# Kernel optimization log

Hardware: AMD Instinct MI355X
Metric: run time of the kernel (lower is better)

## Reference

```python
import jax, jax.numpy as jnp
import numpy as np

B, S, D = 8, 1024, 1024
H = 16
HD = D // H  # 64
FF = 4 * D   # 4096
EPS = 1e-5


def layer_norm(x, g, b):
    mu = jnp.mean(x, axis=-1, keepdims=True)
    var = jnp.mean(jnp.square(x - mu), axis=-1, keepdims=True)
    return (x - mu) * jax.lax.rsqrt(var + EPS) * g + b


def setup_inputs() -> dict:
    key = jax.random.key(0)
    ks = jax.random.split(key, 16)
    s_in = 1.0 / np.sqrt(D)
    s_ff = 1.0 / np.sqrt(FF)
    return {
        "x": jax.random.normal(ks[0], (B, S, D), jnp.float32),
        "ln1_g": jnp.ones((D,), jnp.float32),
        "ln1_b": jnp.zeros((D,), jnp.float32),
        "ln2_g": jnp.ones((D,), jnp.float32),
        "ln2_b": jnp.zeros((D,), jnp.float32),
        # per-head projections stacked on a leading head axis: [H, D, HD]
        "Wq": jax.random.uniform(ks[1], (H, D, HD), jnp.float32, -s_in, s_in),
        "bq": jax.random.uniform(ks[2], (H, HD), jnp.float32, -s_in, s_in),
        "Wk": jax.random.uniform(ks[3], (H, D, HD), jnp.float32, -s_in, s_in),
        "bk": jax.random.uniform(ks[4], (H, HD), jnp.float32, -s_in, s_in),
        "Wv": jax.random.uniform(ks[5], (H, D, HD), jnp.float32, -s_in, s_in),
        "bv": jax.random.uniform(ks[6], (H, HD), jnp.float32, -s_in, s_in),
        "Wo": jax.random.uniform(ks[7], (D, D), jnp.float32, -s_in, s_in),
        "bo": jax.random.uniform(ks[8], (D,), jnp.float32, -s_in, s_in),
        "W1": jax.random.uniform(ks[9], (D, FF), jnp.float32, -s_in, s_in),
        "b1": jax.random.uniform(ks[10], (FF,), jnp.float32, -s_in, s_in),
        "W2": jax.random.uniform(ks[11], (FF, D), jnp.float32, -s_ff, s_ff),
        "b2": jax.random.uniform(ks[12], (D,), jnp.float32, -s_ff, s_ff),
    }


def attention(h, Wq, bq, Wk, bk, Wv, bv, Wo, bo):
    # h: [B,S,D] -> q/k/v: [B,H,S,HD]
    q = jnp.einsum("bsd,hdk->bhsk", h, Wq) + bq[None, :, None, :]
    k = jnp.einsum("bsd,hdk->bhsk", h, Wk) + bk[None, :, None, :]
    v = jnp.einsum("bsd,hdk->bhsk", h, Wv) + bv[None, :, None, :]
    scores = jnp.einsum("bhsk,bhtk->bhst", q, k) / jnp.sqrt(jnp.float32(HD))
    w = jax.nn.softmax(scores, axis=-1)  # [B,H,S,S]
    o = jnp.einsum("bhst,bhtk->bhsk", w, v)
    # concat heads (head order matches torch.cat over per-head outputs)
    o = o.transpose(0, 2, 1, 3).reshape(h.shape[0], h.shape[1], D)
    return o @ Wo + bo


def reference(x, ln1_g, ln1_b, ln2_g, ln2_b, Wq, bq, Wk, bk, Wv, bv, Wo, bo, W1, b1, W2, b2):
    h = layer_norm(x, ln1_g, ln1_b)
    x = x + attention(h, Wq, bq, Wk, bk, Wv, bv, Wo, bo)
    h2 = layer_norm(x, ln2_g, ln2_b)
    ff = jax.nn.gelu(h2 @ W1 + b1, approximate=False) @ W2 + b2  # dropout in eval = identity
    return x + ff
```

## Files before the change

### kernel.cpp

```cpp
#include <hip/hip_runtime.h>
#include <hip/hip_bf16.h>
#include <math.h>

#define DMODEL 1024
#define NH     16
#define HD     64
#define FFDIM  4096
#define SEQ    1024
#define BATCH  8
#define ROWS   (BATCH * SEQ)

typedef __bf16 bf16x8 __attribute__((ext_vector_type(8)));
typedef __bf16 bf16x4 __attribute__((ext_vector_type(4)));
typedef float  f32x4  __attribute__((ext_vector_type(4)));
typedef short  s16x4  __attribute__((ext_vector_type(4)));
typedef unsigned int u32x2 __attribute__((ext_vector_type(2)));

__device__ __forceinline__ unsigned short f2bf(float f) {
  unsigned int u = __builtin_bit_cast(unsigned int, f);
  u += 0x7fff + ((u >> 16) & 1);
  return (unsigned short)(u >> 16);
}

__device__ __forceinline__ unsigned int cvt_pk_bf16(float lo, float hi) {
  unsigned int r;
  asm("v_cvt_pk_bf16_f32 %0, %1, %2" : "=v"(r) : "v"(lo), "v"(hi));
  return r;
}

__device__ __forceinline__ void gload_lds16(const void* g, void* l) {
  __builtin_amdgcn_global_load_lds(
      (const __attribute__((address_space(1))) unsigned int*)g,
      (__attribute__((address_space(3))) unsigned int*)l, 16, 0, 0);
}

__global__ __launch_bounds__(256) void ln_bf16_kernel(
    const float* __restrict__ x, const float* __restrict__ g,
    const float* __restrict__ bta, unsigned short* __restrict__ out) {
  int row = blockIdx.x;
  int tid = threadIdx.x;
  int wid = tid >> 6, lane = tid & 63;
  const float4 v = ((const float4*)(x + (size_t)row * DMODEL))[tid];
  float s = v.x + v.y + v.z + v.w;
#pragma unroll
  for (int off = 32; off >= 1; off >>= 1) s += __shfl_xor(s, off, 64);
  __shared__ float red[8];
  if (lane == 0) red[wid] = s;
  __syncthreads();
  float mu = (red[0] + red[1] + red[2] + red[3]) * (1.0f / DMODEL);
  float4 d;
  d.x = v.x - mu; d.y = v.y - mu; d.z = v.z - mu; d.w = v.w - mu;
  float sq = d.x * d.x + d.y * d.y + d.z * d.z + d.w * d.w;
#pragma unroll
  for (int off = 32; off >= 1; off >>= 1) sq += __shfl_xor(sq, off, 64);
  if (lane == 0) red[4 + wid] = sq;
  __syncthreads();
  float var = (red[4] + red[5] + red[6] + red[7]) * (1.0f / DMODEL);
  float rs = rsqrtf(var + 1e-5f);
  const float4 gg = ((const float4*)g)[tid];
  const float4 bb = ((const float4*)bta)[tid];
  ushort4 o;
  o.x = f2bf(d.x * rs * gg.x + bb.x);
  o.y = f2bf(d.y * rs * gg.y + bb.y);
  o.z = f2bf(d.z * rs * gg.z + bb.z);
  o.w = f2bf(d.w * rs * gg.w + bb.w);
  ((ushort4*)(out + (size_t)row * DMODEL))[tid] = o;
}

__global__ __launch_bounds__(256) void transpose_f2b_kernel(
    const float* __restrict__ in, unsigned short* __restrict__ out,
    int R, int C, long long ibs, long long obs) {
  __shared__ float tile[64][65];
  int b = blockIdx.z;
  int r0 = blockIdx.y * 64, c0 = blockIdx.x * 64;
  const float* ip = in + (size_t)b * ibs;
  unsigned short* op = out + (size_t)b * obs;
  int tid = threadIdx.x;
  int rl = tid >> 4, cl = (tid & 15) * 4;
#pragma unroll
  for (int it = 0; it < 4; ++it) {
    int r = it * 16 + rl;
    float4 v = *(const float4*)(ip + (size_t)(r0 + r) * C + c0 + cl);
    tile[r][cl] = v.x; tile[r][cl + 1] = v.y;
    tile[r][cl + 2] = v.z; tile[r][cl + 3] = v.w;
  }
  __syncthreads();
#pragma unroll
  for (int it = 0; it < 4; ++it) {
    int c = it * 16 + rl;
    ushort4 o;
    o.x = f2bf(tile[cl + 0][c]); o.y = f2bf(tile[cl + 1][c]);
    o.z = f2bf(tile[cl + 2][c]); o.w = f2bf(tile[cl + 3][c]);
    *(ushort4*)(op + (size_t)(c0 + c) * R + r0 + cl) = o;
  }
}

__global__ __launch_bounds__(256) void transpose_qkv_kernel(
    const float* __restrict__ Wq, const float* __restrict__ Wk,
    const float* __restrict__ Wv, unsigned short* __restrict__ out) {
  __shared__ float tile[64][65];
  int z = blockIdx.z;
  int wsel = z >> 4, head = z & 15;
  const float* base = (wsel == 0) ? Wq : (wsel == 1) ? Wk : Wv;
  const float* ip = base + (size_t)head * 65536;
  unsigned short* op = out + (size_t)z * 65536;
  int r0 = blockIdx.y * 64;
  int tid = threadIdx.x;
  int rl = tid >> 4, cl = (tid & 15) * 4;
#pragma unroll
  for (int it = 0; it < 4; ++it) {
    int r = it * 16 + rl;
    float4 v = *(const float4*)(ip + (size_t)(r0 + r) * 64 + cl);
    tile[r][cl] = v.x; tile[r][cl + 1] = v.y;
    tile[r][cl + 2] = v.z; tile[r][cl + 3] = v.w;
  }
  __syncthreads();
#pragma unroll
  for (int it = 0; it < 4; ++it) {
    int c = it * 16 + rl;
    ushort4 o;
    o.x = f2bf(tile[cl + 0][c]); o.y = f2bf(tile[cl + 1][c]);
    o.z = f2bf(tile[cl + 2][c]); o.w = f2bf(tile[cl + 3][c]);
    *(ushort4*)(op + (size_t)c * 1024 + r0 + cl) = o;
  }
}

__global__ __launch_bounds__(256) void transpose_v_kernel(
    const unsigned short* __restrict__ V, unsigned short* __restrict__ Vt) {
  __shared__ unsigned short tile[64][68];
  int bh = blockIdx.y;
  int b = bh >> 4, h = bh & 15;
  int t0 = blockIdx.x * 64;
  int tid = threadIdx.x;
  int rl = tid >> 4, cl = (tid & 15) * 4;
  const unsigned short* ip = V + ((size_t)(b * SEQ + t0)) * DMODEL + h * HD;
#pragma unroll
  for (int it = 0; it < 4; ++it) {
    int t = it * 16 + rl;
    ushort4 v = *(const ushort4*)(ip + (size_t)t * DMODEL + cl);
    tile[t][cl] = v.x; tile[t][cl + 1] = v.y;
    tile[t][cl + 2] = v.z; tile[t][cl + 3] = v.w;
  }
  __syncthreads();
  unsigned short* op = Vt + ((size_t)bh * HD) * SEQ + t0;
#pragma unroll
  for (int it = 0; it < 4; ++it) {
    int d = it * 16 + rl;
    ushort4 o;
    o.x = tile[cl + 0][d]; o.y = tile[cl + 1][d];
    o.z = tile[cl + 2][d]; o.w = tile[cl + 3][d];
    *(ushort4*)(op + (size_t)d * SEQ + cl) = o;
  }
}

#define QSCALE 0.18033688f

template <int EPI>
__global__ __launch_bounds__(512, 4) void gemmdb_kernel(
    const unsigned short* __restrict__ A, const unsigned short* __restrict__ Bt,
    const float* __restrict__ bias, const float* __restrict__ resid,
    unsigned short* __restrict__ outb, float* __restrict__ outf,
    int M, int N, int K, int NX) {
  __shared__ __align__(16) unsigned short As[2 * 128 * 64];
  __shared__ __align__(16) unsigned short Bs[2 * 128 * 64];

  const int tid = threadIdx.x;
  const int wid = tid >> 6, lane = tid & 63;
  const int l15 = lane & 15, l4 = lane >> 4;
  const int wm = wid >> 1, wn = wid & 1;

  const int id = (int)blockIdx.x;
  const int xcd = id & 7, j = id >> 3;
  const int w = j >> 6, l = j & 63;
  const int spx = (int)gridDim.x >> 9;
  const int nbx8 = NX >> 3;
  const int g = xcd * spx + w;
  const int by = (g / nbx8) * 8 + (l >> 3);
  const int bx = (g % nbx8) * 8 + (l & 7);

  const size_t KBY = (size_t)K * 2;

  const int rS = tid >> 3;
  const int cS = ((tid & 7) ^ (rS & 7)) << 4;
  const char* gA = (const char*)A + (size_t)(by * 128 + rS) * KBY + cS;
  const char* gB = (const char*)Bt + (size_t)(bx * 128 + rS) * KBY + cS;
  char* sA = (char*)As + tid * 16;
  char* sB = (char*)Bs + tid * 16;

  const int rsw = (l4 ^ (l15 & 7)) << 4;
  const char* aRd0 = (const char*)As + (wm * 32 + l15) * 128 + rsw;
  const char* aRd1 = (const char*)As + (wm * 32 + l15) * 128 + (rsw ^ 64);
  const char* bRd0 = (const char*)Bs + (wn * 64 + l15) * 128 + rsw;
  const char* bRd1 = (const char*)Bs + (wn * 64 + l15) * 128 + (rsw ^ 64);

  f32x4 acc[2][4];
  const f32x4 fz = {0.f, 0.f, 0.f, 0.f};
#pragma unroll
  for (int i = 0; i < 2; ++i)
#pragma unroll
    for (int j2 = 0; j2 < 4; ++j2) acc[i][j2] = fz;

  const int nt = K >> 6;

  gload_lds16(gA, sA);
  gload_lds16(gA + 64 * KBY, sA + 8192);
  gload_lds16(gB, sB);
  gload_lds16(gB + 64 * KBY, sB + 8192);
  asm volatile("s_waitcnt vmcnt(0)" ::: "memory");
  __builtin_amdgcn_sched_barrier(0);
  __builtin_amdgcn_s_barrier();
  __builtin_amdgcn_sched_barrier(0);

#pragma unroll 1
  for (int t = 0; t < nt; ++t) {
    const int cur = t & 1;
    if (t + 1 < nt) {
      const size_t ko = (size_t)(t + 1) << 7;
      const int nb = (cur ^ 1) << 14;
      gload_lds16(gA + ko, sA + nb);
      gload_lds16(gA + 64 * KBY + ko, sA + nb + 8192);
      gload_lds16(gB + ko, sB + nb);
      gload_lds16(gB + 64 * KBY + ko, sB + nb + 8192);
    }
    const int off = cur << 14;
#pragma unroll
    for (int kk = 0; kk < 2; ++kk) {
      const char* aR = (kk ? aRd1 : aRd0) + off;
      const char* bR = (kk ? bRd1 : bRd0) + off;
      bf16x8 afr[2], bfr[4];
#pragma unroll
      for (int ni = 0; ni < 4; ++ni) bfr[ni] = *(const bf16x8*)(bR + ni * 2048);
#pragma unroll
      for (int mi = 0; mi < 2; ++mi) afr[mi] = *(const bf16x8*)(aR + mi * 2048);
      __builtin_amdgcn_s_setprio(1);
#pragma unroll
      for (int mi = 0; mi < 2; ++mi)
#pragma unroll
        for (int ni = 0; ni < 4; ++ni)
          acc[mi][ni] = __builtin_amdgcn_mfma_f32_16x16x32_bf16(
              afr[mi], bfr[ni], acc[mi][ni], 0, 0, 0);
      __builtin_amdgcn_s_setprio(0);
    }
    asm volatile("s_waitcnt vmcnt(0)" ::: "memory");
    __builtin_amdgcn_sched_barrier(0);
    __builtin_amdgcn_s_barrier();
    __builtin_amdgcn_sched_barrier(0);
  }

#pragma unroll
  for (int mi = 0; mi < 2; ++mi) {
#pragma unroll
    for (int ni = 0; ni < 4; ++ni) {
      int col = bx * 128 + wn * 64 + ni * 16 + l15;
      float bn = bias[col];
#pragma unroll
      for (int jj = 0; jj < 4; ++jj) {
        int row = by * 128 + wm * 32 + mi * 16 + l4 * 4 + jj;
        float v = acc[mi][ni][jj] + bn;
        if (EPI == 1) {
          outf[(size_t)row * N + col] = v + resid[(size_t)row * N + col];
        } else {
          outb[(size_t)row * N + col] = f2bf(v);
        }
      }
    }
  }
}

template <int EPI>
__global__ __launch_bounds__(512, 2) void gemmbig_kernel(
    const unsigned short* __restrict__ A, const unsigned short* __restrict__ Bt,
    const float* __restrict__ bias, const float* __restrict__ bias2,
    const float* __restrict__ bias3,
    unsigned short* __restrict__ outb, unsigned short* __restrict__ outb2,
    unsigned short* __restrict__ outb3,
    int M, int N, int K, int YPX) {
  __shared__ __align__(16) unsigned short As[2 * 256 * 64];
  __shared__ __align__(16) unsigned short Bs[2 * 256 * 64];

  const int tid = threadIdx.x;
  const int wid = tid >> 6, lane = tid & 63;
  const int l15 = lane & 15, l4 = lane >> 4;
  const int wm = wid >> 2, wn = wid & 3;

  const int id = (int)blockIdx.x;
  const int xcd = id & 7, i0 = id >> 3;
  const int by = xcd * YPX + (i0 % YPX);
  const int bx = i0 / YPX;

  const size_t KBY = (size_t)K * 2;

  const int rS = tid >> 3;
  const int cS = ((tid & 7) ^ (rS & 7)) << 4;
  const char* gA = (const char*)A + (size_t)(by * 256 + rS) * KBY + cS;
  const char* gB = (const char*)Bt + (size_t)(bx * 256 + rS) * KBY + cS;
  char* sA = (char*)As + tid * 16;
  char* sB = (char*)Bs + tid * 16;

  const int rsw = (l4 ^ (l15 & 7)) << 4;
  const char* aRd0 = (const char*)As + (wm * 128 + l15) * 128 + rsw;
  const char* aRd1 = (const char*)As + (wm * 128 + l15) * 128 + (rsw ^ 64);
  const char* bRd0 = (const char*)Bs + (wn * 64 + l15) * 128 + rsw;
  const char* bRd1 = (const char*)Bs + (wn * 64 + l15) * 128 + (rsw ^ 64);

  f32x4 acc[8][4];
  const f32x4 fz = {0.f, 0.f, 0.f, 0.f};
#pragma unroll
  for (int i = 0; i < 8; ++i)
#pragma unroll
    for (int n = 0; n < 4; ++n) acc[i][n] = fz;

  const int nt = K >> 6;

#define STAGE8(NB, KO)                                                       \
  do {                                                                       \
    gload_lds16(gA + (KO), sA + (NB));                                       \
    gload_lds16(gA + 64 * KBY + (KO), sA + (NB) + 8192);                     \
    gload_lds16(gA + 128 * KBY + (KO), sA + (NB) + 16384);                   \
    gload_lds16(gA + 192 * KBY + (KO), sA + (NB) + 24576);                   \
    gload_lds16(gB + (KO), sB + (NB));                                       \
    gload_lds16(gB + 64 * KBY + (KO), sB + (NB) + 8192);                     \
    gload_lds16(gB + 128 * KBY + (KO), sB + (NB) + 16384);                   \
    gload_lds16(gB + 192 * KBY + (KO), sB + (NB) + 24576);                   \
  } while (0)

  STAGE8(0, 0);
  asm volatile("s_waitcnt vmcnt(0)" ::: "memory");
  __builtin_amdgcn_sched_barrier(0);
  __builtin_amdgcn_s_barrier();
  __builtin_amdgcn_sched_barrier(0);

#pragma unroll 1
  for (int t = 0; t < nt; ++t) {
    const int cur = t & 1;
    if (t + 1 < nt) STAGE8((cur ^ 1) << 15, (size_t)(t + 1) << 7);
    const int off = cur << 15;
#pragma unroll
    for (int kk = 0; kk < 2; ++kk) {
      const char* aR = (kk ? aRd1 : aRd0) + off;
      const char* bR = (kk ? bRd1 : bRd0) + off;
      bf16x8 av[8], bv[4];
#pragma unroll
      for (int ni = 0; ni < 4; ++ni) bv[ni] = *(const bf16x8*)(bR + ni * 2048);
#pragma unroll
      for (int mi = 0; mi < 8; ++mi) av[mi] = *(const bf16x8*)(aR + mi * 2048);
      __builtin_amdgcn_s_setprio(1);
#pragma unroll
      for (int mi = 0; mi < 8; ++mi)
#pragma unroll
        for (int ni = 0; ni < 4; ++ni)
          acc[mi][ni] = __builtin_amdgcn_mfma_f32_16x16x32_bf16(
              av[mi], bv[ni], acc[mi][ni], 0, 0, 0);
      __builtin_amdgcn_s_setprio(0);
    }
    asm volatile("s_waitcnt vmcnt(0)" ::: "memory");
    __builtin_amdgcn_sched_barrier(0);
    __builtin_amdgcn_s_barrier();
    __builtin_amdgcn_sched_barrier(0);
  }

  if (EPI == 5) {
    const int range = bx >> 2;
    const float* bp = (range == 0) ? bias : (range == 1) ? bias2 : bias3;
    unsigned short* op = (range == 0) ? outb : (range == 1) ? outb2 : outb3;
    const float scale = (range == 0) ? QSCALE : 1.0f;
#pragma unroll
    for (int mi = 0; mi < 8; ++mi) {
#pragma unroll
      for (int ni = 0; ni < 4; ++ni) {
        int colL = (bx & 3) * 256 + wn * 64 + ni * 16 + l15;
        float bn = bp[colL];
#pragma unroll
        for (int jj = 0; jj < 4; ++jj) {
          int row = by * 256 + wm * 128 + mi * 16 + l4 * 4 + jj;
          op[(size_t)row * 1024 + colL] = f2bf((acc[mi][ni][jj] + bn) * scale);
        }
      }
    }
  } else {
#pragma unroll
    for (int mi = 0; mi < 8; ++mi) {
#pragma unroll
      for (int ni = 0; ni < 4; ++ni) {
        int col = bx * 256 + wn * 64 + ni * 16 + l15;
        float bn = bias[col];
#pragma unroll
        for (int jj = 0; jj < 4; ++jj) {
          int row = by * 256 + wm * 128 + mi * 16 + l4 * 4 + jj;
          float v = acc[mi][ni][jj] + bn;
          float gel = 0.5f * v * (1.0f + erff(v * 0.70710678118f));
          outb[(size_t)row * N + col] = f2bf(gel);
        }
      }
    }
  }
#undef STAGE8
}

__global__ __launch_bounds__(256, 3) void attn_kernel(
    const unsigned short* __restrict__ Q, const unsigned short* __restrict__ K,
    const unsigned short* __restrict__ Vt, unsigned short* __restrict__ O) {
  __shared__ __align__(16) unsigned short Ks[128 * 64];
  __shared__ __align__(16) unsigned short Vs[64 * 128];
  int tid = threadIdx.x, wid = tid >> 6, lane = tid & 63;
  int l15 = lane & 15, l4 = lane >> 4;
  int sid = blockIdx.x;
  int aid = (sid & 7) * 256 + (sid >> 3);
  int bh = aid >> 4, qb = aid & 15;
  int b = bh >> 4, h = bh & 15;
  int q0 = qb * 64 + wid * 16;
  const f32x4 fz = {0.f, 0.f, 0.f, 0.f};

  const unsigned short* Qbase = Q + ((size_t)(b * SEQ + q0)) * DMODEL + h * HD;
  bf16x8 qf[2];
#pragma unroll
  for (int kh = 0; kh < 2; ++kh)
    qf[kh] = *(const bf16x8*)(Qbase + (size_t)l15 * DMODEL + kh * 32 + l4 * 8);

  f32x4 o[4];
#pragma unroll
  for (int i = 0; i < 4; ++i) o[i] = fz;
  float mrun = -1e30f, lrun = 0.0f;

  const unsigned short* Kb = K + (size_t)b * SEQ * DMODEL + h * HD;
  const unsigned short* Vb = Vt + (size_t)bh * HD * SEQ;
  int krow = tid >> 3, kchunk = tid & 7;
  int vrow = tid >> 4, vchunk = tid & 15;

  for (int t0 = 0; t0 < SEQ; t0 += 128) {
    __syncthreads();
#pragma unroll
    for (int p = 0; p < 4; ++p) {
      int kr = p * 32 + krow;
      int kg = kchunk ^ (kr & 7);
      gload_lds16(Kb + (size_t)(t0 + kr) * DMODEL + kg * 8,
                  (char*)Ks + p * 4096 + tid * 16);
      int vr = p * 16 + vrow;
      int vg = vchunk ^ (vr & 7);
      gload_lds16(Vb + (size_t)vr * SEQ + t0 + vg * 8,
                  (char*)Vs + p * 4096 + tid * 16);
    }
    __syncthreads();
    f32x4 s[8];
#pragma unroll
    for (int ts = 0; ts < 8; ++ts) {
      int row = ts * 16 + l15;
      bf16x8 k0f = *(const bf16x8*)((const char*)Ks + row * 128 + ((l4) ^ (row & 7)) * 16);
      bf16x8 k1f = *(const bf16x8*)((const char*)Ks + row * 128 + ((4 + l4) ^ (row & 7)) * 16);
      s[ts] = __builtin_amdgcn_mfma_f32_16x16x32_bf16(k0f, qf[0], fz, 0, 0, 0);
      s[ts] = __builtin_amdgcn_mfma_f32_16x16x32_bf16(k1f, qf[1], s[ts], 0, 0, 0);
    }
    float tsm[8];
#pragma unroll
    for (int ts = 0; ts < 8; ++ts)
      tsm[ts] = fmaxf(fmaxf(s[ts][0], s[ts][1]), fmaxf(s[ts][2], s[ts][3]));
    float tm = fmaxf(fmaxf(fmaxf(tsm[0], tsm[1]), fmaxf(tsm[2], tsm[3])),
                     fmaxf(fmaxf(tsm[4], tsm[5]), fmaxf(tsm[6], tsm[7])));
    tm = fmaxf(tm, __shfl_xor(tm, 16, 64));
    tm = fmaxf(tm, __shfl_xor(tm, 32, 64));
    if (!__all(tm - mrun <= 8.0f)) {
      float mnew = fmaxf(mrun, tm);
      float alpha = __builtin_amdgcn_exp2f(mrun - mnew);
      lrun *= alpha;
      float a0 = __shfl(alpha, l4 * 4 + 0, 64);
      float a1 = __shfl(alpha, l4 * 4 + 1, 64);
      float a2 = __shfl(alpha, l4 * 4 + 2, 64);
      float a3 = __shfl(alpha, l4 * 4 + 3, 64);
#pragma unroll
      for (int d = 0; d < 4; ++d) {
        o[d][0] *= a0; o[d][1] *= a1; o[d][2] *= a2; o[d][3] *= a3;
      }
      mrun = mnew;
    }
    unsigned int pk[8][2];
    float ps = 0.0f;
#pragma unroll
    for (int ts = 0; ts < 8; ++ts) {
      float e0 = __builtin_amdgcn_exp2f(s[ts][0] - mrun);
      float e1 = __builtin_amdgcn_exp2f(s[ts][1] - mrun);
      float e2 = __builtin_amdgcn_exp2f(s[ts][2] - mrun);
      float e3 = __builtin_amdgcn_exp2f(s[ts][3] - mrun);
      ps += (e0 + e1) + (e2 + e3);
      pk[ts][0] = cvt_pk_bf16(e0, e1);
      pk[ts][1] = cvt_pk_bf16(e2, e3);
    }
    ps += __shfl_xor(ps, 16, 64);
    ps += __shfl_xor(ps, 32, 64);
    lrun += ps;
#pragma unroll
    for (int ts = 0; ts < 8; ++ts) {
      s16x4 pf = __builtin_bit_cast(s16x4, (u32x2){pk[ts][0], pk[ts][1]});
#pragma unroll
      for (int d = 0; d < 4; ++d) {
        int vr = d * 16 + l15;
        int chunk = 2 * ts + (l4 >> 1);
        int phys = chunk ^ (vr & 7);
        s16x4 vf = *(const s16x4*)((const char*)Vs + vr * 256 + phys * 16 +
                                   (l4 & 1) * 8);
        o[d] = __builtin_amdgcn_mfma_f32_16x16x16bf16_1k(pf, vf, o[d], 0, 0, 0);
      }
    }
  }
  unsigned short* Ob = O + ((size_t)(b * SEQ + q0)) * DMODEL + h * HD;
  float inv = 1.0f / lrun;
  float i0 = __shfl(inv, l4 * 4 + 0, 64);
  float i1 = __shfl(inv, l4 * 4 + 1, 64);
  float i2 = __shfl(inv, l4 * 4 + 2, 64);
  float i3 = __shfl(inv, l4 * 4 + 3, 64);
#pragma unroll
  for (int d = 0; d < 4; ++d) {
    Ob[(size_t)(l4 * 4 + 0) * DMODEL + d * 16 + l15] = f2bf(o[d][0] * i0);
    Ob[(size_t)(l4 * 4 + 1) * DMODEL + d * 16 + l15] = f2bf(o[d][1] * i1);
    Ob[(size_t)(l4 * 4 + 2) * DMODEL + d * 16 + l15] = f2bf(o[d][2] * i2);
    Ob[(size_t)(l4 * 4 + 3) * DMODEL + d * 16 + l15] = f2bf(o[d][3] * i3);
  }
}

extern "C" void kernel_launch(void* const* d_in, const int* in_sizes, int n_in,
                              void* d_out, int out_size, void* d_ws, size_t ws_size,
                              hipStream_t stream) {
  (void)in_sizes; (void)n_in; (void)out_size; (void)ws_size;
  const float* x    = (const float*)d_in[0];
  const float* ln1g = (const float*)d_in[1];
  const float* ln1b = (const float*)d_in[2];
  const float* ln2g = (const float*)d_in[3];
  const float* ln2b = (const float*)d_in[4];
  const float* Wq   = (const float*)d_in[5];
  const float* bq   = (const float*)d_in[6];
  const float* Wk   = (const float*)d_in[7];
  const float* bk   = (const float*)d_in[8];
  const float* Wv   = (const float*)d_in[9];
  const float* bv   = (const float*)d_in[10];
  const float* Wo   = (const float*)d_in[11];
  const float* bo   = (const float*)d_in[12];
  const float* W1   = (const float*)d_in[13];
  const float* b1   = (const float*)d_in[14];
  const float* W2   = (const float*)d_in[15];
  const float* b2   = (const float*)d_in[16];
  float* out = (float*)d_out;

  char* ws = (char*)d_ws;
  const size_t MB = 1u << 20;
  unsigned short* wqT = (unsigned short*)(ws + 0 * MB);
  unsigned short* woT = (unsigned short*)(ws + 6 * MB);
  unsigned short* w1T = (unsigned short*)(ws + 8 * MB);
  unsigned short* w2T = (unsigned short*)(ws + 16 * MB);
  unsigned short* hb  = (unsigned short*)(ws + 24 * MB);
  unsigned short* Qb  = (unsigned short*)(ws + 40 * MB);
  unsigned short* Kb  = (unsigned short*)(ws + 56 * MB);
  unsigned short* Vb  = (unsigned short*)(ws + 72 * MB);
  unsigned short* Vt  = (unsigned short*)(ws + 88 * MB);
  unsigned short* Ob  = Vb;
  unsigned short* ff1 = (unsigned short*)(ws + 40 * MB);

  transpose_qkv_kernel<<<dim3(1, 16, 48), 256, 0, stream>>>(Wq, Wk, Wv, wqT);
  transpose_f2b_kernel<<<dim3(16, 16, 1), 256, 0, stream>>>(Wo, woT, 1024, 1024, 0, 0);
  transpose_f2b_kernel<<<dim3(64, 16, 1), 256, 0, stream>>>(W1, w1T, 1024, 4096, 0, 0);
  transpose_f2b_kernel<<<dim3(16, 64, 1), 256, 0, stream>>>(W2, w2T, 4096, 1024, 0, 0);

  ln_bf16_kernel<<<dim3(ROWS), 256, 0, stream>>>(x, ln1g, ln1b, hb);

  gemmbig_kernel<5><<<dim3(384), 512, 0, stream>>>(
      hb, wqT, bq, bk, bv, Qb, Kb, Vb, ROWS, 1024, DMODEL, 4);

  transpose_v_kernel<<<dim3(16, 128), 256, 0, stream>>>(Vb, Vt);

  attn_kernel<<<dim3(2048), 256, 0, stream>>>(Qb, Kb, Vt, Ob);

  gemmdb_kernel<1><<<dim3(512), 512, 0, stream>>>(
      Ob, woT, bo, x, nullptr, out, ROWS, DMODEL, DMODEL, 8);

  ln_bf16_kernel<<<dim3(ROWS), 256, 0, stream>>>(out, ln2g, ln2b, hb);

  gemmbig_kernel<2><<<dim3(512), 512, 0, stream>>>(
      hb, w1T, b1, nullptr, nullptr, ff1, nullptr, nullptr,
      ROWS, FFDIM, DMODEL, 4);

  gemmdb_kernel<1><<<dim3(512), 512, 0, stream>>>(
      ff1, w2T, b2, out, nullptr, out, ROWS, DMODEL, FFDIM, 8);
}
```

Measured before the change: 374.2 us.

## Move QKV GEMM to 128-tile kernel and halve K-step in FF1 GEMM

The fused QKV projection now runs on the 128x128 double-buffered GEMM kernel with 1536 blocks instead of the 256x256 kernel with 384 blocks, so the grid covers the GPU more evenly. The big 256x256 kernel, now used only for FF1 with GELU, stages 32-wide K slices instead of 64, halving LDS use to allow more resident blocks, with a new swizzle. The cost is more K iterations and barriers per tile, and less operand reuse for the QKV GEMM.

Result: no change. 376.7 us (+0.7%).

```diff
diff --git a/kernel.cpp b/kernel.cpp
--- a/kernel.cpp
+++ b/kernel.cpp
@@ -158,8 +158,10 @@
 template <int EPI>
 __global__ __launch_bounds__(512, 4) void gemmdb_kernel(
     const unsigned short* __restrict__ A, const unsigned short* __restrict__ Bt,
-    const float* __restrict__ bias, const float* __restrict__ resid,
-    unsigned short* __restrict__ outb, float* __restrict__ outf,
+    const float* __restrict__ bias, const float* __restrict__ bias2,
+    const float* __restrict__ bias3, const float* __restrict__ resid,
+    unsigned short* __restrict__ outb, unsigned short* __restrict__ outb2,
+    unsigned short* __restrict__ outb3, float* __restrict__ outf,
     int M, int N, int K, int NX) {
   __shared__ __align__(16) unsigned short As[2 * 128 * 64];
   __shared__ __align__(16) unsigned short Bs[2 * 128 * 64];
@@ -247,36 +249,55 @@
     __builtin_amdgcn_sched_barrier(0);
   }
 
-#pragma unroll
-  for (int mi = 0; mi < 2; ++mi) {
-#pragma unroll
-    for (int ni = 0; ni < 4; ++ni) {
-      int col = bx * 128 + wn * 64 + ni * 16 + l15;
-      float bn = bias[col];
-#pragma unroll
-      for (int jj = 0; jj < 4; ++jj) {
-        int row = by * 128 + wm * 32 + mi * 16 + l4 * 4 + jj;
-        float v = acc[mi][ni][jj] + bn;
-        if (EPI == 1) {
-          outf[(size_t)row * N + col] = v + resid[(size_t)row * N + col];
-        } else {
-          outb[(size_t)row * N + col] = f2bf(v);
+  if (EPI == 5) {
+    const int range = bx >> 3;
+    const float* bp = (range == 0) ? bias : (range == 1) ? bias2 : bias3;
+    unsigned short* op = (range == 0) ? outb : (range == 1) ? outb2 : outb3;
+    const float scale = (range == 0) ? QSCALE : 1.0f;
+#pragma unroll
+    for (int mi = 0; mi < 2; ++mi) {
+#pragma unroll
+      for (int ni = 0; ni < 4; ++ni) {
+        int colL = (bx & 7) * 128 + wn * 64 + ni * 16 + l15;
+        float bn = bp[colL];
+#pragma unroll
+        for (int jj = 0; jj < 4; ++jj) {
+          int row = by * 128 + wm * 32 + mi * 16 + l4 * 4 + jj;
+          op[(size_t)row * 1024 + colL] = f2bf((acc[mi][ni][jj] + bn) * scale);
         }
       }
     }
-  }
-}
-
-template <int EPI>
-__global__ __launch_bounds__(512, 2) void gemmbig_kernel(
+  } else {
+#pragma unroll
+    for (int mi = 0; mi < 2; ++mi) {
+#pragma unroll
+      for (int ni = 0; ni < 4; ++ni) {
+        int col = bx * 128 + wn * 64 + ni * 16 + l15;
+        float bn = bias[col];
+#pragma unroll
+        for (int jj = 0; jj < 4; ++jj) {
+          int row = by * 128 + wm * 32 + mi * 16 + l4 * 4 + jj;
+          float v = acc[mi][ni][jj] + bn;
+          if (EPI == 1) {
+            outf[(size_t)row * N + col] = v + resid[(size_t)row * N + col];
+          } else if (EPI == 2) {
+            float gel = 0.5f * v * (1.0f + erff(v * 0.70710678118f));
+            outb[(size_t)row * N + col] = f2bf(gel);
+          } else {
+            outb[(size_t)row * N + col] = f2bf(v);
+          }
+        }
+      }
+    }
+  }
+}
+
+__global__ __launch_bounds__(512, 2) void gemmbig2_kernel(
     const unsigned short* __restrict__ A, const unsigned short* __restrict__ Bt,
-    const float* __restrict__ bias, const float* __restrict__ bias2,
-    const float* __restrict__ bias3,
-    unsigned short* __restrict__ outb, unsigned short* __restrict__ outb2,
-    unsigned short* __restrict__ outb3,
+    const float* __restrict__ bias, unsigned short* __restrict__ outb,
     int M, int N, int K, int YPX) {
-  __shared__ __align__(16) unsigned short As[2 * 256 * 64];
-  __shared__ __align__(16) unsigned short Bs[2 * 256 * 64];
+  __shared__ __align__(16) unsigned short As[2 * 256 * 32];
+  __shared__ __align__(16) unsigned short Bs[2 * 256 * 32];
 
   const int tid = threadIdx.x;
   const int wid = tid >> 6, lane = tid & 63;
@@ -290,18 +311,16 @@
 
   const size_t KBY = (size_t)K * 2;
 
-  const int rS = tid >> 3;
-  const int cS = ((tid & 7) ^ (rS & 7)) << 4;
+  const int rS = tid >> 2;
+  const int cS = ((tid & 3) ^ ((rS >> 1) & 3)) << 4;
   const char* gA = (const char*)A + (size_t)(by * 256 + rS) * KBY + cS;
   const char* gB = (const char*)Bt + (size_t)(bx * 256 + rS) * KBY + cS;
   char* sA = (char*)As + tid * 16;
   char* sB = (char*)Bs + tid * 16;
 
-  const int rsw = (l4 ^ (l15 & 7)) << 4;
-  const char* aRd0 = (const char*)As + (wm * 128 + l15) * 128 + rsw;
-  const char* aRd1 = (const char*)As + (wm * 128 + l15) * 128 + (rsw ^ 64);
-  const char* bRd0 = (const char*)Bs + (wn * 64 + l15) * 128 + rsw;
-  const char* bRd1 = (const char*)Bs + (wn * 64 + l15) * 128 + (rsw ^ 64);
+  const int fsw = (l4 ^ ((l15 >> 1) & 3)) << 4;
+  const char* aRd = (const char*)As + (wm * 128 + l15) * 64 + fsw;
+  const char* bRd = (const char*)Bs + (wn * 64 + l15) * 64 + fsw;
 
   f32x4 acc[8][4];
   const f32x4 fz = {0.f, 0.f, 0.f, 0.f};
@@ -310,21 +329,17 @@
 #pragma unroll
     for (int n = 0; n < 4; ++n) acc[i][n] = fz;
 
-  const int nt = K >> 6;
-
-#define STAGE8(NB, KO)                                                       \
-  do {                                                                       \
-    gload_lds16(gA + (KO), sA + (NB));                                       \
-    gload_lds16(gA + 64 * KBY + (KO), sA + (NB) + 8192);                     \
-    gload_lds16(gA + 128 * KBY + (KO), sA + (NB) + 16384);                   \
-    gload_lds16(gA + 192 * KBY + (KO), sA + (NB) + 24576);                   \
-    gload_lds16(gB + (KO), sB + (NB));                                       \
-    gload_lds16(gB + 64 * KBY + (KO), sB + (NB) + 8192);                     \
-    gload_lds16(gB + 128 * KBY + (KO), sB + (NB) + 16384);                   \
-    gload_lds16(gB + 192 * KBY + (KO), sB + (NB) + 24576);                   \
+  const int nt = K >> 5;
+
+#define STG2(NB, KO)                                                        \
+  do {                                                                      \
+    gload_lds16(gA + (KO), sA + (NB));                                      \
+    gload_lds16(gA + 128 * KBY + (KO), sA + (NB) + 8192);                   \
+    gload_lds16(gB + (KO), sB + (NB));                                      \
+    gload_lds16(gB + 128 * KBY + (KO), sB + (NB) + 8192);                   \
   } while (0)
 
-  STAGE8(0, 0);
+  STG2(0, 0);
   asm volatile("s_waitcnt vmcnt(0)" ::: "memory");
   __builtin_amdgcn_sched_barrier(0);
   __builtin_amdgcn_s_barrier();
@@ -333,17 +348,16 @@
 #pragma unroll 1
   for (int t = 0; t < nt; ++t) {
     const int cur = t & 1;
-    if (t + 1 < nt) STAGE8((cur ^ 1) << 15, (size_t)(t + 1) << 7);
-    const int off = cur << 15;
-#pragma unroll
-    for (int kk = 0; kk < 2; ++kk) {
-      const char* aR = (kk ? aRd1 : aRd0) + off;
-      const char* bR = (kk ? bRd1 : bRd0) + off;
+    if (t + 1 < nt) STG2((cur ^ 1) << 14, (size_t)(t + 1) << 6);
+    const int off = cur << 14;
+    {
+      const char* aB = aRd + off;
+      const char* bB = bRd + off;
       bf16x8 av[8], bv[4];
 #pragma unroll
-      for (int ni = 0; ni < 4; ++ni) bv[ni] = *(const bf16x8*)(bR + ni * 2048);
-#pragma unroll
-      for (int mi = 0; mi < 8; ++mi) av[mi] = *(const bf16x8*)(aR + mi * 2048);
+      for (int ni = 0; ni < 4; ++ni) bv[ni] = *(const bf16x8*)(bB + ni * 1024);
+#pragma unroll
+      for (int mi = 0; mi < 8; ++mi) av[mi] = *(const bf16x8*)(aB + mi * 1024);
       __builtin_amdgcn_s_setprio(1);
 #pragma unroll
       for (int mi = 0; mi < 8; ++mi)
@@ -359,42 +373,22 @@
     __builtin_amdgcn_sched_barrier(0);
   }
 
-  if (EPI == 5) {
-    const int range = bx >> 2;
-    const float* bp = (range == 0) ? bias : (range == 1) ? bias2 : bias3;
-    unsigned short* op = (range == 0) ? outb : (range == 1) ? outb2 : outb3;
-    const float scale = (range == 0) ? QSCALE : 1.0f;
-#pragma unroll
-    for (int mi = 0; mi < 8; ++mi) {
-#pragma unroll
-      for (int ni = 0; ni < 4; ++ni) {
-        int colL = (bx & 3) * 256 + wn * 64 + ni * 16 + l15;
-        float bn = bp[colL];
-#pragma unroll
-        for (int jj = 0; jj < 4; ++jj) {
-          int row = by * 256 + wm * 128 + mi * 16 + l4 * 4 + jj;
-          op[(size_t)row * 1024 + colL] = f2bf((acc[mi][ni][jj] + bn) * scale);
-        }
+#pragma unroll
+  for (int mi = 0; mi < 8; ++mi) {
+#pragma unroll
+    for (int ni = 0; ni < 4; ++ni) {
+      int col = bx * 256 + wn * 64 + ni * 16 + l15;
+      float bn = bias[col];
+#pragma unroll
+      for (int jj = 0; jj < 4; ++jj) {
+        int row = by * 256 + wm * 128 + mi * 16 + l4 * 4 + jj;
+        float v = acc[mi][ni][jj] + bn;
+        float gel = 0.5f * v * (1.0f + erff(v * 0.70710678118f));
+        outb[(size_t)row * N + col] = f2bf(gel);
       }
     }
-  } else {
-#pragma unroll
-    for (int mi = 0; mi < 8; ++mi) {
-#pragma unroll
-      for (int ni = 0; ni < 4; ++ni) {
-        int col = bx * 256 + wn * 64 + ni * 16 + l15;
-        float bn = bias[col];
-#pragma unroll
-        for (int jj = 0; jj < 4; ++jj) {
-          int row = by * 256 + wm * 128 + mi * 16 + l4 * 4 + jj;
-          float v = acc[mi][ni][jj] + bn;
-          float gel = 0.5f * v * (1.0f + erff(v * 0.70710678118f));
-          outb[(size_t)row * N + col] = f2bf(gel);
-        }
-      }
-    }
-  }
-#undef STAGE8
+  }
+#undef STG2
 }
 
 __global__ __launch_bounds__(256, 3) void attn_kernel(
@@ -560,22 +554,23 @@
 
   ln_bf16_kernel<<<dim3(ROWS), 256, 0, stream>>>(x, ln1g, ln1b, hb);
 
-  gemmbig_kernel<5><<<dim3(384), 512, 0, stream>>>(
-      hb, wqT, bq, bk, bv, Qb, Kb, Vb, ROWS, 1024, DMODEL, 4);
+  gemmdb_kernel<5><<<dim3(1536), 512, 0, stream>>>(
+      hb, wqT, bq, bk, bv, nullptr, Qb, Kb, Vb, nullptr, ROWS, 1024, DMODEL, 24);
 
   transpose_v_kernel<<<dim3(16, 128), 256, 0, stream>>>(Vb, Vt);
 
   attn_kernel<<<dim3(2048), 256, 0, stream>>>(Qb, Kb, Vt, Ob);
 
   gemmdb_kernel<1><<<dim3(512), 512, 0, stream>>>(
-      Ob, woT, bo, x, nullptr, out, ROWS, DMODEL, DMODEL, 8);
+      Ob, woT, bo, nullptr, nullptr, x, nullptr, nullptr, nullptr, out,
+      ROWS, DMODEL, DMODEL, 8);
 
   ln_bf16_kernel<<<dim3(ROWS), 256, 0, stream>>>(out, ln2g, ln2b, hb);
 
-  gemmbig_kernel<2><<<dim3(512), 512, 0, stream>>>(
-      hb, w1T, b1, nullptr, nullptr, ff1, nullptr, nullptr,
-      ROWS, FFDIM, DMODEL, 4);
+  gemmbig2_kernel<<<dim3(512), 512, 0, stream>>>(
+      hb, w1T, b1, ff1, ROWS, FFDIM, DMODEL, 4);
 
   gemmdb_kernel<1><<<dim3(512), 512, 0, stream>>>(
-      ff1, w2T, b2, out, nullptr, out, ROWS, DMODEL, FFDIM, 8);
-}
+      ff1, w2T, b2, nullptr, nullptr, out, nullptr, nullptr, nullptr, out,
+      ROWS, DMODEL, FFDIM, 8);
+}
```
